# Optimization experiments

Measured on AMD Instinct MI355X. Metric: run time of the kernel, lower is better.

Reference implementation:

```python
import jax, jax.numpy as jnp
import numpy as np

EMBED_DIM = 1024
BATCH = 4
SEQ = 2048


def setup_inputs() -> dict:
    key = jax.random.key(0)
    ks = jax.random.split(key, 9)
    E = EMBED_DIM
    s = 1.0 / np.sqrt(E)
    inp = {
        "x": jax.random.normal(ks[0], (BATCH, SEQ, E), dtype=jnp.float32),
        "Wq": jax.random.uniform(ks[1], (E, E), jnp.float32, -s, s),
        "bq": jax.random.uniform(ks[2], (E,), jnp.float32, -s, s),
        "Wk": jax.random.uniform(ks[3], (E, E), jnp.float32, -s, s),
        "bk": jax.random.uniform(ks[4], (E,), jnp.float32, -s, s),
        "Wv": jax.random.uniform(ks[5], (E, E), jnp.float32, -s, s),
        "bv": jax.random.uniform(ks[6], (E,), jnp.float32, -s, s),
        "Wo": jax.random.uniform(ks[7], (E, E), jnp.float32, -s, s),
        "bo": jax.random.uniform(ks[8], (E,), jnp.float32, -s, s),
    }
    return inp


def reference(x, Wq, bq, Wk, bk, Wv, bv, Wo, bo):
    # x: [B, S, E]. Single-head attention over full embed_dim.
    scale = x.shape[-1] ** -0.5
    q = jnp.einsum("bse,ef->bsf", x, Wq.T) + bq
    k = jnp.einsum("bse,ef->bsf", x, Wk.T) + bk
    v = jnp.einsum("bse,ef->bsf", x, Wv.T) + bv
    scores = jnp.einsum("bqe,bke->bqk", q, k) * scale  # [B, S, S]
    attn = jax.nn.softmax(scores, axis=-1)             # dropout p=0 -> identity
    out = jnp.einsum("bqk,bke->bqe", attn, v)
    return jnp.einsum("bse,ef->bsf", out, Wo.T) + bo
```

## Files before the change

kernel.cpp:

```cpp
#include <hip/hip_runtime.h>
#include <hip/hip_bf16.h>


typedef __bf16 bf16_t;
typedef __bf16 bf16x8 __attribute__((ext_vector_type(8)));
typedef __bf16 bf16x4 __attribute__((ext_vector_type(4)));
typedef float  f32x4  __attribute__((ext_vector_type(4)));

__device__ __forceinline__ void async_copy16(const void* g, void* l) {
  __builtin_amdgcn_global_load_lds(
      (const __attribute__((address_space(1))) void*)g,
      (__attribute__((address_space(3))) void*)l, 16, 0, 0);
}

__device__ __forceinline__ void store_out(float* p, float v)  { *p = v; }
__device__ __forceinline__ void store_out(bf16_t* p, float v) { *p = (bf16_t)v; }

#define BM 128
#define BN 128
#define BKT 64

template <typename OutT, bool HasBias>
__global__ __launch_bounds__(256) void gemm_bt(
    const bf16_t* __restrict__ A, const bf16_t* __restrict__ B,
    OutT* __restrict__ C, const float* __restrict__ bias,
    int M, int N, int K, float scale,
    long long strideA, long long strideB, long long strideC) {
  const int z = blockIdx.z;
  A += (long long)z * strideA;
  B += (long long)z * strideB;
  C += (long long)z * strideC;

  __shared__ __align__(16) bf16_t As[BM * BKT];
  __shared__ __align__(16) bf16_t Bs[BN * BKT];

  const int t    = threadIdx.x;
  const int lane = t & 63;
  const int w    = t >> 6;
  const int wm   = w & 1;
  const int wn   = w >> 1;
  const int tileM = blockIdx.y * BM;
  const int tileN = blockIdx.x * BN;

  f32x4 acc[4][4] = {};

  for (int k0 = 0; k0 < K; k0 += BKT) {
#pragma unroll
    for (int i = 0; i < 4; ++i) {
      const int c   = t + 256 * i;
      const int row = c >> 3;
      const int cc  = c & 7;
      const int gcc = cc ^ (row & 7);
      const int ldsbase = ((t & ~63) + 256 * i) * 8;
      const bf16_t* ga = A + (long long)(tileM + row) * K + k0 + gcc * 8;
      async_copy16(ga, &As[ldsbase]);
      const bf16_t* gb = B + (long long)(tileN + row) * K + k0 + gcc * 8;
      async_copy16(gb, &Bs[ldsbase]);
    }
    __syncthreads();

#pragma unroll
    for (int s = 0; s < 2; ++s) {
      bf16x8 af[4], bfr[4];
      const int kc = s * 4 + (lane >> 4);
#pragma unroll
      for (int ti = 0; ti < 4; ++ti) {
        const int row = wm * 64 + ti * 16 + (lane & 15);
        const int off = row * BKT + ((kc ^ (row & 7)) * 8);
        af[ti] = *(const bf16x8*)&As[off];
      }
#pragma unroll
      for (int tj = 0; tj < 4; ++tj) {
        const int row = wn * 64 + tj * 16 + (lane & 15);
        const int off = row * BKT + ((kc ^ (row & 7)) * 8);
        bfr[tj] = *(const bf16x8*)&Bs[off];
      }
#pragma unroll
      for (int ti = 0; ti < 4; ++ti)
#pragma unroll
        for (int tj = 0; tj < 4; ++tj)
          acc[ti][tj] = __builtin_amdgcn_mfma_f32_16x16x32_bf16(
              af[ti], bfr[tj], acc[ti][tj], 0, 0, 0);
    }
    __syncthreads();
  }

#pragma unroll
  for (int tj = 0; tj < 4; ++tj) {
    const int col = tileN + wn * 64 + tj * 16 + (lane & 15);
    const float bv = HasBias ? bias[col] : 0.f;
#pragma unroll
    for (int ti = 0; ti < 4; ++ti) {
      const int row0 = tileM + wm * 64 + ti * 16 + (lane >> 4) * 4;
#pragma unroll
      for (int r = 0; r < 4; ++r) {
        const float v = acc[ti][tj][r] * scale + bv;
        store_out(&C[(long long)(row0 + r) * N + col], v);
      }
    }
  }
}

__global__ __launch_bounds__(256) void cast_f32_bf16(
    const float4* __restrict__ in, bf16x4* __restrict__ out, int n4) {
  const int i = blockIdx.x * 256 + threadIdx.x;
  if (i >= n4) return;
  const float4 v = in[i];
  bf16x4 o;
  o[0] = (bf16_t)v.x; o[1] = (bf16_t)v.y; o[2] = (bf16_t)v.z; o[3] = (bf16_t)v.w;
  out[i] = o;
}

__global__ __launch_bounds__(256) void transpose_bf16(
    const bf16_t* __restrict__ in, bf16_t* __restrict__ out, int R, int C) {
  const long long base = (long long)blockIdx.z * R * C;
  in += base; out += base;
  __shared__ bf16_t tile[32][33];
  const int tx = threadIdx.x, ty = threadIdx.y;
  const int x = blockIdx.x * 32 + tx;
  const int y0 = blockIdx.y * 32;
#pragma unroll
  for (int j = 0; j < 32; j += 8)
    tile[ty + j][tx] = in[(long long)(y0 + ty + j) * C + x];
  __syncthreads();
  const int x2 = y0 + tx;
  const int y2 = blockIdx.x * 32;
#pragma unroll
  for (int j = 0; j < 32; j += 8)
    out[(long long)(y2 + ty + j) * R + x2] = tile[tx][ty + j];
}

__global__ __launch_bounds__(256) void softmax_rows(
    const bf16_t* __restrict__ S, bf16_t* __restrict__ P, int cols) {
  const long long row = blockIdx.x;
  const bf16x8* inp = (const bf16x8*)(S + row * cols);
  bf16x8* outp      = (bf16x8*)(P + row * cols);
  const int t = threadIdx.x;
  const int w = t >> 6, lane = t & 63;

  const bf16x8 v = inp[t];
  float f[8];
#pragma unroll
  for (int j = 0; j < 8; ++j) f[j] = (float)v[j];

  float m = f[0];
#pragma unroll
  for (int j = 1; j < 8; ++j) m = fmaxf(m, f[j]);
#pragma unroll
  for (int off = 32; off > 0; off >>= 1) m = fmaxf(m, __shfl_xor(m, off));

  __shared__ float red[8];
  if (lane == 0) red[w] = m;
  __syncthreads();
  m = fmaxf(fmaxf(red[0], red[1]), fmaxf(red[2], red[3]));

  float e[8], sum = 0.f;
#pragma unroll
  for (int j = 0; j < 8; ++j) { e[j] = __expf(f[j] - m); sum += e[j]; }
#pragma unroll
  for (int off = 32; off > 0; off >>= 1) sum += __shfl_xor(sum, off);
  if (lane == 0) red[4 + w] = sum;
  __syncthreads();
  sum = red[4] + red[5] + red[6] + red[7];

  const float inv = 1.f / sum;
  bf16x8 o;
#pragma unroll
  for (int j = 0; j < 8; ++j) o[j] = (bf16_t)(e[j] * inv);
  outp[t] = o;
}

extern "C" void kernel_launch(void* const* d_in, const int* in_sizes, int n_in,
                              void* d_out, int out_size, void* d_ws, size_t ws_size,
                              hipStream_t stream) {
  const int E = 1024, S = 2048, B = 4;
  const int BS = B * S;

  const float* x  = (const float*)d_in[0];
  const float* Wq = (const float*)d_in[1];
  const float* bq = (const float*)d_in[2];
  const float* Wk = (const float*)d_in[3];
  const float* bk = (const float*)d_in[4];
  const float* Wv = (const float*)d_in[5];
  const float* bv = (const float*)d_in[6];
  const float* Wo = (const float*)d_in[7];
  const float* bo = (const float*)d_in[8];
  float* out = (float*)d_out;

  char* w = (char*)d_ws;
  const size_t MB = 1ull << 20;
  bf16_t* Wqb = (bf16_t*)(w + 0 * MB);
  bf16_t* Wkb = (bf16_t*)(w + 2 * MB);
  bf16_t* Wvb = (bf16_t*)(w + 4 * MB);
  bf16_t* Wob = (bf16_t*)(w + 6 * MB);
  bf16_t* xb  = (bf16_t*)(w + 8 * MB);
  bf16_t* Qb  = (bf16_t*)(w + 24 * MB);
  bf16_t* Kb  = (bf16_t*)(w + 40 * MB);
  bf16_t* Vb  = (bf16_t*)(w + 56 * MB);
  bf16_t* VTb = (bf16_t*)(w + 72 * MB);
  bf16_t* Sb  = (bf16_t*)(w + 88 * MB);
  bf16_t* Pb  = (bf16_t*)(w + 8 * MB);
  bf16_t* Ob  = (bf16_t*)(w + 56 * MB);

  {
    const int n4w = E * E / 4;
    const int gw = (n4w + 255) / 256;
    cast_f32_bf16<<<gw, 256, 0, stream>>>((const float4*)Wq, (bf16x4*)Wqb, n4w);
    cast_f32_bf16<<<gw, 256, 0, stream>>>((const float4*)Wk, (bf16x4*)Wkb, n4w);
    cast_f32_bf16<<<gw, 256, 0, stream>>>((const float4*)Wv, (bf16x4*)Wvb, n4w);
    cast_f32_bf16<<<gw, 256, 0, stream>>>((const float4*)Wo, (bf16x4*)Wob, n4w);
    const int n4x = BS * E / 4;
    cast_f32_bf16<<<(n4x + 255) / 256, 256, 0, stream>>>((const float4*)x, (bf16x4*)xb, n4x);
  }

  {
    dim3 g(E / BN, BS / BM, 1);
    gemm_bt<bf16_t, true><<<g, 256, 0, stream>>>(xb, Wqb, Qb, bq, BS, E, E, 1.f, 0, 0, 0);
    gemm_bt<bf16_t, true><<<g, 256, 0, stream>>>(xb, Wkb, Kb, bk, BS, E, E, 1.f, 0, 0, 0);
    gemm_bt<bf16_t, true><<<g, 256, 0, stream>>>(xb, Wvb, Vb, bv, BS, E, E, 1.f, 0, 0, 0);
  }

  {
    dim3 g(E / 32, S / 32, B);
    transpose_bf16<<<g, dim3(32, 8), 0, stream>>>(Vb, VTb, S, E);
  }

  {
    dim3 g(S / BN, S / BM, B);
    gemm_bt<bf16_t, false><<<g, 256, 0, stream>>>(
        Qb, Kb, Sb, nullptr, S, S, E, 0.03125f,
        (long long)S * E, (long long)S * E, (long long)S * S);
  }

  softmax_rows<<<BS, 256, 0, stream>>>(Sb, Pb, S);

  {
    dim3 g(E / BN, S / BM, B);
    gemm_bt<bf16_t, false><<<g, 256, 0, stream>>>(
        Pb, VTb, Ob, nullptr, S, E, S, 1.f,
        (long long)S * S, (long long)E * S, (long long)S * E);
  }

  {
    dim3 g(E / BN, BS / BM, 1);
    gemm_bt<float, true><<<g, 256, 0, stream>>>(Ob, Wob, out, bo, BS, E, E, 1.f, 0, 0, 0);
  }
}
```

Measured before the change: 322.7 us.

## Fuse QKV projections into one GEMM and switch to 32x32x16 MFMA

The Q, K and V projections become a single GEMM against a concatenated [3E, E] weight, with strided lda/ldb/ldc so the attention GEMMs and the V transpose read directly from the interleaved QKV buffer. The four weight casts are merged into one launch. The GEMM inner loop moves from 16x16x32 MFMA tiles to 32x32x16 tiles, which cuts LDS fragment loads per MFMA. The goal is fewer launches, less re-reading of x, and higher MFMA efficiency. The cost is strided QKV accesses and a new accumulator layout in the epilogue stores.

Result: faster. 296.2 us (-8.2%).

```diff
diff --git a/kernel.cpp b/kernel.cpp
--- a/kernel.cpp
+++ b/kernel.cpp
@@ -5,7 +5,7 @@
 typedef __bf16 bf16_t;
 typedef __bf16 bf16x8 __attribute__((ext_vector_type(8)));
 typedef __bf16 bf16x4 __attribute__((ext_vector_type(4)));
-typedef float  f32x4  __attribute__((ext_vector_type(4)));
+typedef float  f32x16 __attribute__((ext_vector_type(16)));
 
 __device__ __forceinline__ void async_copy16(const void* g, void* l) {
   __builtin_amdgcn_global_load_lds(
@@ -20,11 +20,13 @@
 #define BN 128
 #define BKT 64
 
-template <typename OutT, bool HasBias>
+template <typename OutT, int NBIAS>
 __global__ __launch_bounds__(256) void gemm_bt(
     const bf16_t* __restrict__ A, const bf16_t* __restrict__ B,
-    OutT* __restrict__ C, const float* __restrict__ bias,
-    int M, int N, int K, float scale,
+    OutT* __restrict__ C,
+    const float* __restrict__ b0, const float* __restrict__ b1,
+    const float* __restrict__ b2,
+    int M, int N, int K, int lda, int ldb, int ldc, float scale,
     long long strideA, long long strideB, long long strideC) {
   const int z = blockIdx.z;
   A += (long long)z * strideA;
@@ -42,7 +44,7 @@
   const int tileM = blockIdx.y * BM;
   const int tileN = blockIdx.x * BN;
 
-  f32x4 acc[4][4] = {};
+  f32x16 acc[2][2] = {};
 
   for (int k0 = 0; k0 < K; k0 += BKT) {
 #pragma unroll
@@ -52,53 +54,68 @@
       const int cc  = c & 7;
       const int gcc = cc ^ (row & 7);
       const int ldsbase = ((t & ~63) + 256 * i) * 8;
-      const bf16_t* ga = A + (long long)(tileM + row) * K + k0 + gcc * 8;
-      async_copy16(ga, &As[ldsbase]);
-      const bf16_t* gb = B + (long long)(tileN + row) * K + k0 + gcc * 8;
-      async_copy16(gb, &Bs[ldsbase]);
+      async_copy16(A + (long long)(tileM + row) * lda + k0 + gcc * 8, &As[ldsbase]);
+      async_copy16(B + (long long)(tileN + row) * ldb + k0 + gcc * 8, &Bs[ldsbase]);
     }
     __syncthreads();
 
 #pragma unroll
-    for (int s = 0; s < 2; ++s) {
-      bf16x8 af[4], bfr[4];
-      const int kc = s * 4 + (lane >> 4);
-#pragma unroll
-      for (int ti = 0; ti < 4; ++ti) {
-        const int row = wm * 64 + ti * 16 + (lane & 15);
-        const int off = row * BKT + ((kc ^ (row & 7)) * 8);
-        af[ti] = *(const bf16x8*)&As[off];
+    for (int s = 0; s < 4; ++s) {
+      const int kc = s * 2 + (lane >> 5);
+      bf16x8 af[2], bfr[2];
+#pragma unroll
+      for (int ti = 0; ti < 2; ++ti) {
+        const int row = wm * 64 + ti * 32 + (lane & 31);
+        af[ti] = *(const bf16x8*)&As[row * BKT + ((kc ^ (row & 7)) * 8)];
       }
 #pragma unroll
-      for (int tj = 0; tj < 4; ++tj) {
-        const int row = wn * 64 + tj * 16 + (lane & 15);
-        const int off = row * BKT + ((kc ^ (row & 7)) * 8);
-        bfr[tj] = *(const bf16x8*)&Bs[off];
+      for (int tj = 0; tj < 2; ++tj) {
+        const int row = wn * 64 + tj * 32 + (lane & 31);
+        bfr[tj] = *(const bf16x8*)&Bs[row * BKT + ((kc ^ (row & 7)) * 8)];
       }
 #pragma unroll
-      for (int ti = 0; ti < 4; ++ti)
-#pragma unroll
-        for (int tj = 0; tj < 4; ++tj)
-          acc[ti][tj] = __builtin_amdgcn_mfma_f32_16x16x32_bf16(
+      for (int ti = 0; ti < 2; ++ti)
+#pragma unroll
+        for (int tj = 0; tj < 2; ++tj)
+          acc[ti][tj] = __builtin_amdgcn_mfma_f32_32x32x16_bf16(
               af[ti], bfr[tj], acc[ti][tj], 0, 0, 0);
     }
     __syncthreads();
   }
 
 #pragma unroll
-  for (int tj = 0; tj < 4; ++tj) {
-    const int col = tileN + wn * 64 + tj * 16 + (lane & 15);
-    const float bv = HasBias ? bias[col] : 0.f;
-#pragma unroll
-    for (int ti = 0; ti < 4; ++ti) {
-      const int row0 = tileM + wm * 64 + ti * 16 + (lane >> 4) * 4;
-#pragma unroll
-      for (int r = 0; r < 4; ++r) {
-        const float v = acc[ti][tj][r] * scale + bv;
-        store_out(&C[(long long)(row0 + r) * N + col], v);
+  for (int tj = 0; tj < 2; ++tj) {
+    const int col = tileN + wn * 64 + tj * 32 + (lane & 31);
+    float bv = 0.f;
+    if (NBIAS == 1) bv = b0[col];
+    if (NBIAS == 3) {
+      const float* bp = col < 1024 ? b0 : (col < 2048 ? b1 : b2);
+      bv = bp[col & 1023];
+    }
+#pragma unroll
+    for (int ti = 0; ti < 2; ++ti) {
+      const int rowb = tileM + wm * 64 + ti * 32 + 4 * (lane >> 5);
+#pragma unroll
+      for (int r = 0; r < 16; ++r) {
+        const int row = rowb + (r & 3) + 8 * (r >> 2);
+        store_out(&C[(long long)row * ldc + col], acc[ti][tj][r] * scale + bv);
       }
     }
   }
+}
+
+__global__ __launch_bounds__(256) void cast_weights(
+    const float4* __restrict__ w0, const float4* __restrict__ w1,
+    const float4* __restrict__ w2, const float4* __restrict__ w3,
+    bf16x4* __restrict__ dst, int n4) {
+  const int z = blockIdx.z;
+  const float4* src = z == 0 ? w0 : (z == 1 ? w1 : (z == 2 ? w2 : w3));
+  const int i = blockIdx.x * 256 + threadIdx.x;
+  if (i >= n4) return;
+  const float4 v = src[i];
+  bf16x4 o;
+  o[0] = (bf16_t)v.x; o[1] = (bf16_t)v.y; o[2] = (bf16_t)v.z; o[3] = (bf16_t)v.w;
+  dst[(long long)z * n4 + i] = o;
 }
 
 __global__ __launch_bounds__(256) void cast_f32_bf16(
@@ -112,16 +129,17 @@
 }
 
 __global__ __launch_bounds__(256) void transpose_bf16(
-    const bf16_t* __restrict__ in, bf16_t* __restrict__ out, int R, int C) {
-  const long long base = (long long)blockIdx.z * R * C;
-  in += base; out += base;
+    const bf16_t* __restrict__ in, bf16_t* __restrict__ out, int R, int C,
+    int ldin, long long sIn, long long sOut) {
+  in  += (long long)blockIdx.z * sIn;
+  out += (long long)blockIdx.z * sOut;
   __shared__ bf16_t tile[32][33];
   const int tx = threadIdx.x, ty = threadIdx.y;
   const int x = blockIdx.x * 32 + tx;
   const int y0 = blockIdx.y * 32;
 #pragma unroll
   for (int j = 0; j < 32; j += 8)
-    tile[ty + j][tx] = in[(long long)(y0 + ty + j) * C + x];
+    tile[ty + j][tx] = in[(long long)(y0 + ty + j) * ldin + x];
   __syncthreads();
   const int x2 = y0 + tx;
   const int y2 = blockIdx.x * 32;
@@ -189,60 +207,43 @@
 
   char* w = (char*)d_ws;
   const size_t MB = 1ull << 20;
-  bf16_t* Wqb = (bf16_t*)(w + 0 * MB);
-  bf16_t* Wkb = (bf16_t*)(w + 2 * MB);
-  bf16_t* Wvb = (bf16_t*)(w + 4 * MB);
-  bf16_t* Wob = (bf16_t*)(w + 6 * MB);
-  bf16_t* xb  = (bf16_t*)(w + 8 * MB);
-  bf16_t* Qb  = (bf16_t*)(w + 24 * MB);
-  bf16_t* Kb  = (bf16_t*)(w + 40 * MB);
-  bf16_t* Vb  = (bf16_t*)(w + 56 * MB);
-  bf16_t* VTb = (bf16_t*)(w + 72 * MB);
-  bf16_t* Sb  = (bf16_t*)(w + 88 * MB);
-  bf16_t* Pb  = (bf16_t*)(w + 8 * MB);
-  bf16_t* Ob  = (bf16_t*)(w + 56 * MB);
-
-  {
-    const int n4w = E * E / 4;
-    const int gw = (n4w + 255) / 256;
-    cast_f32_bf16<<<gw, 256, 0, stream>>>((const float4*)Wq, (bf16x4*)Wqb, n4w);
-    cast_f32_bf16<<<gw, 256, 0, stream>>>((const float4*)Wk, (bf16x4*)Wkb, n4w);
-    cast_f32_bf16<<<gw, 256, 0, stream>>>((const float4*)Wv, (bf16x4*)Wvb, n4w);
-    cast_f32_bf16<<<gw, 256, 0, stream>>>((const float4*)Wo, (bf16x4*)Wob, n4w);
-    const int n4x = BS * E / 4;
-    cast_f32_bf16<<<(n4x + 255) / 256, 256, 0, stream>>>((const float4*)x, (bf16x4*)xb, n4x);
-  }
-
-  {
-    dim3 g(E / BN, BS / BM, 1);
-    gemm_bt<bf16_t, true><<<g, 256, 0, stream>>>(xb, Wqb, Qb, bq, BS, E, E, 1.f, 0, 0, 0);
-    gemm_bt<bf16_t, true><<<g, 256, 0, stream>>>(xb, Wkb, Kb, bk, BS, E, E, 1.f, 0, 0, 0);
-    gemm_bt<bf16_t, true><<<g, 256, 0, stream>>>(xb, Wvb, Vb, bv, BS, E, E, 1.f, 0, 0, 0);
-  }
-
-  {
-    dim3 g(E / 32, S / 32, B);
-    transpose_bf16<<<g, dim3(32, 8), 0, stream>>>(Vb, VTb, S, E);
-  }
-
-  {
-    dim3 g(S / BN, S / BM, B);
-    gemm_bt<bf16_t, false><<<g, 256, 0, stream>>>(
-        Qb, Kb, Sb, nullptr, S, S, E, 0.03125f,
-        (long long)S * E, (long long)S * E, (long long)S * S);
-  }
+  bf16_t* Wqkvb = (bf16_t*)(w + 0 * MB);
+  bf16_t* Wob   = Wqkvb + 3 * E * E;
+  bf16_t* xb    = (bf16_t*)(w + 8 * MB);
+  bf16_t* QKVb  = (bf16_t*)(w + 24 * MB);
+  bf16_t* VTb   = (bf16_t*)(w + 72 * MB);
+  bf16_t* Sb    = (bf16_t*)(w + 88 * MB);
+  bf16_t* Pb    = (bf16_t*)(w + 8 * MB);
+  bf16_t* Ob    = (bf16_t*)(w + 40 * MB);
+
+  const int n4w = E * E / 4;
+  cast_weights<<<dim3((n4w + 255) / 256, 1, 4), 256, 0, stream>>>(
+      (const float4*)Wq, (const float4*)Wk, (const float4*)Wv, (const float4*)Wo,
+      (bf16x4*)Wqkvb, n4w);
+  const int n4x = BS * E / 4;
+  cast_f32_bf16<<<(n4x + 255) / 256, 256, 0, stream>>>(
+      (const float4*)x, (bf16x4*)xb, n4x);
+
+  gemm_bt<bf16_t, 3><<<dim3(3 * E / BN, BS / BM, 1), 256, 0, stream>>>(
+      xb, Wqkvb, QKVb, bq, bk, bv,
+      BS, 3 * E, E, E, E, 3 * E, 1.f, 0, 0, 0);
+
+  transpose_bf16<<<dim3(E / 32, S / 32, B), dim3(32, 8), 0, stream>>>(
+      QKVb + 2 * E, VTb, S, E, 3 * E, (long long)S * 3 * E, (long long)E * S);
+
+  gemm_bt<bf16_t, 0><<<dim3(S / BN, S / BM, B), 256, 0, stream>>>(
+      QKVb, QKVb + E, Sb, nullptr, nullptr, nullptr,
+      S, S, E, 3 * E, 3 * E, S, 0.03125f,
+      (long long)S * 3 * E, (long long)S * 3 * E, (long long)S * S);
 
   softmax_rows<<<BS, 256, 0, stream>>>(Sb, Pb, S);
 
-  {
-    dim3 g(E / BN, S / BM, B);
-    gemm_bt<bf16_t, false><<<g, 256, 0, stream>>>(
-        Pb, VTb, Ob, nullptr, S, E, S, 1.f,
-        (long long)S * S, (long long)E * S, (long long)S * E);
-  }
-
-  {
-    dim3 g(E / BN, BS / BM, 1);
-    gemm_bt<float, true><<<g, 256, 0, stream>>>(Ob, Wob, out, bo, BS, E, E, 1.f, 0, 0, 0);
-  }
-}
+  gemm_bt<bf16_t, 0><<<dim3(E / BN, S / BM, B), 256, 0, stream>>>(
+      Pb, VTb, Ob, nullptr, nullptr, nullptr,
+      S, E, S, S, S, E, 1.f,
+      (long long)S * S, (long long)E * S, (long long)S * E);
+
+  gemm_bt<float, 1><<<dim3(E / BN, BS / BM, 1), 256, 0, stream>>>(
+      Ob, Wob, out, bo, nullptr, nullptr,
+      BS, E, E, E, E, E, 1.f, 0, 0, 0);
+}
```
